# Kernel tuning notes

Hardware: AMD Instinct MI355X
Metric: run time of the kernel (lower is better)

The kernel has to match this reference:

```python
import jax, jax.numpy as jnp
import numpy as np

N_EMBD = 1024
N_HEAD = 16
HEAD_DIM = N_EMBD // N_HEAD
SEQ = 2048
BATCH = 2
WINDOW = 256
SCALE = 1.0 / np.sqrt(HEAD_DIM)
MASK_VALUE = -10000.0


def setup_inputs() -> dict:
    key = jax.random.key(0)
    ks = jax.random.split(key, 5)
    s = 0.02
    return {
        "hidden_states": jax.random.normal(ks[0], (BATCH, SEQ, N_EMBD), dtype=jnp.float32),
        "w_attn": jax.random.normal(ks[1], (N_EMBD, 3 * N_EMBD), dtype=jnp.float32) * s,
        "b_attn": jnp.zeros((3 * N_EMBD,), dtype=jnp.float32),
        "w_proj": jax.random.normal(ks[2], (N_EMBD, N_EMBD), dtype=jnp.float32) * s,
        "b_proj": jnp.zeros((N_EMBD,), dtype=jnp.float32),
    }


def _mask(seq_len):
    # causal AND sliding window: j <= i and j > i - WINDOW
    i = jnp.arange(seq_len)[:, None]
    j = jnp.arange(seq_len)[None, :]
    return (j <= i) & (j > i - WINDOW)  # [T, T] bool


def reference(hidden_states, w_attn, b_attn, w_proj, b_proj):
    B, T, _ = hidden_states.shape
    qkv = hidden_states @ w_attn + b_attn  # [B, T, 3E]
    q, k, v = jnp.split(qkv, 3, axis=-1)
    # [B, H, T, D]
    q = q.reshape(B, T, N_HEAD, HEAD_DIM).transpose(0, 2, 1, 3)
    k = k.reshape(B, T, N_HEAD, HEAD_DIM).transpose(0, 2, 1, 3)
    v = v.reshape(B, T, N_HEAD, HEAD_DIM).transpose(0, 2, 1, 3)

    scores = jnp.einsum("bhqd,bhkd->bhqk", q, k) * SCALE  # [B, H, T, T]
    mask = _mask(T)[None, None]  # [1, 1, T, T]
    scores = jnp.where(mask, scores, MASK_VALUE)
    scores = jnp.clip(scores, -10000.0, 10000.0)
    attn = jax.nn.softmax(scores, axis=-1)
    out = jnp.einsum("bhqk,bhkd->bhqd", attn, v)  # [B, H, T, D]
    out = out.transpose(0, 2, 1, 3).reshape(B, T, N_EMBD)
    return out @ w_proj + b_proj
```

## Files before the change

### kernel.cpp

```cpp
#include <hip/hip_runtime.h>


typedef __bf16 bf16_t;
typedef bf16_t bf16x8 __attribute__((ext_vector_type(8)));
typedef bf16_t bf16x4 __attribute__((ext_vector_type(4)));
typedef float  floatx4 __attribute__((ext_vector_type(4)));

#define SEQ_T   2048
#define NHEAD   16
#define HDIM    64
#define EMB     1024
#define WIN     256
#define SCALE_F 0.125f

__device__ __forceinline__ int detect_bf16(const uint4* __restrict__ det)
{
    const int lane = threadIdx.x & 63;
    const uint4 v = det[lane];
    int c = 0;
    #pragma unroll
    for (int e = 0; e < 4; ++e) {
        const unsigned int ex = ((&v.x)[e] >> 7) & 0xffu;
        c += (ex >= 100u && ex <= 150u) ? 1 : 0;
    }
    #pragma unroll
    for (int m = 32; m >= 1; m >>= 1) c += __shfl_xor(c, m, 64);
    return (c * 2 > 256) ? 1 : 0;
}

__global__ __launch_bounds__(256) void prologue(
    const void* __restrict__ hidden, bf16_t* __restrict__ Hc,
    const void* __restrict__ ba, bf16_t* __restrict__ bba,
    const void* __restrict__ bp, bf16_t* __restrict__ bbp,
    const void* __restrict__ wA, bf16_t* __restrict__ WtA,
    const void* __restrict__ wP, bf16_t* __restrict__ WtP)
{
    __shared__ __align__(16) bf16_t tile[64][68];
    const int f = detect_bf16((const uint4*)hidden);
    const int blk = blockIdx.x;

    if (blk < 4100) {
        if (f) return;
        const float* src;
        bf16_t* dst;
        int base;
        if (blk < 4096)      { src = (const float*)hidden; dst = Hc;  base = blk * 1024; }
        else if (blk < 4099) { src = (const float*)ba;     dst = bba; base = (blk - 4096) * 1024; }
        else                 { src = (const float*)bp;     dst = bbp; base = 0; }
        const int i4 = base + threadIdx.x * 4;
        const float4 x = *(const float4*)(src + i4);
        bf16x4 v;
        v[0] = (bf16_t)x.x; v[1] = (bf16_t)x.y;
        v[2] = (bf16_t)x.z; v[3] = (bf16_t)x.w;
        *(bf16x4*)(dst + i4) = v;
        return;
    }

    int id = blk - 4100;
    const void* W; bf16_t* Wt; int N, bx, by;
    if (id < 768) { W = wA; Wt = WtA; N = 3072; bx = id % 48; by = id / 48; }
    else { id -= 768; W = wP; Wt = WtP; N = 1024; bx = id % 16; by = id / 16; }
    const int K = 1024;
    const int n0 = bx * 64;
    const int k0 = by * 64;
    const int tx = threadIdx.x & 15;
    const int ty = threadIdx.x >> 4;

    #pragma unroll
    for (int r = ty; r < 64; r += 16) {
        bf16x4 v;
        const size_t base = (size_t)(k0 + r) * N + n0 + tx * 4;
        if (f) {
            v = *(const bf16x4*)((const bf16_t*)W + base);
        } else {
            const float4 x = *(const float4*)((const float*)W + base);
            v[0] = (bf16_t)x.x; v[1] = (bf16_t)x.y;
            v[2] = (bf16_t)x.z; v[3] = (bf16_t)x.w;
        }
        *(bf16x4*)&tile[r][tx * 4] = v;
    }
    __syncthreads();
    #pragma unroll
    for (int r = ty; r < 64; r += 16) {
        bf16x4 v;
        v[0] = tile[tx * 4 + 0][r];
        v[1] = tile[tx * 4 + 1][r];
        v[2] = tile[tx * 4 + 2][r];
        v[3] = tile[tx * 4 + 3][r];
        *(bf16x4*)(Wt + (size_t)(n0 + r) * K + k0 + tx * 4) = v;
    }
}

template<int BNt, int BKt>
__global__ __launch_bounds__(256, 2) void gemm_bt_bias(
    const bf16_t* __restrict__ Abf,
    const bf16_t* __restrict__ Aalt,
    const bf16_t* __restrict__ Bt,
    const bf16_t* __restrict__ biasbf,
    const bf16_t* __restrict__ biasalt,
    void* __restrict__ C,
    int M, int N, int K,
    int force_bf16, const uint4* __restrict__ det)
{
    constexpr int BMt = 128;
    constexpr int NF  = BNt / 32;
    constexpr int LPR = BKt / 8;
    constexpr int CM  = LPR - 1;
    constexpr int RPL = 64 / LPR;
    constexpr int SL  = BKt / 32;
    __shared__ __align__(16) bf16_t As[2][BMt * BKt];
    __shared__ __align__(16) bf16_t Bs[2][BNt * BKt];

    const int flag = detect_bf16(det);
    const bf16_t* A    = flag ? Abf    : Aalt;
    const bf16_t* bias = flag ? biasbf : biasalt;
    const int obf = force_bf16 | flag;

    const int tid  = threadIdx.x;
    const int wave = tid >> 6;
    const int lane = tid & 63;
    const int quad = lane >> 4;
    const int n16  = lane & 15;
    const int m0 = blockIdx.y * BMt;
    const int n0 = blockIdx.x * BNt;
    const int wm = (wave >> 1) * 64;
    const int wn = (wave & 1) * (BNt / 2);

    floatx4 acc[4][NF] = {};

    const int lr   = lane / LPR;
    const int lc16 = lane % LPR;

    auto stage = [&](int bsel, int k0) {
        #pragma unroll
        for (int t = 0; t < (BMt / 4) / RPL; ++t) {
            const int row0 = wave * (BMt / 4) + t * RPL;
            const int g = (lc16 ^ ((row0 + lr) & CM)) * 8;
            const bf16_t* ga = A + (size_t)(m0 + row0 + lr) * K + k0 + g;
            __builtin_amdgcn_global_load_lds(
                (const __attribute__((address_space(1))) void*)ga,
                (__attribute__((address_space(3))) void*)(As[bsel] + row0 * BKt),
                16, 0, 0);
        }
        #pragma unroll
        for (int t = 0; t < (BNt / 4) / RPL; ++t) {
            const int row0 = wave * (BNt / 4) + t * RPL;
            const int g = (lc16 ^ ((row0 + lr) & CM)) * 8;
            const bf16_t* gb = Bt + (size_t)(n0 + row0 + lr) * K + k0 + g;
            __builtin_amdgcn_global_load_lds(
                (const __attribute__((address_space(1))) void*)gb,
                (__attribute__((address_space(3))) void*)(Bs[bsel] + row0 * BKt),
                16, 0, 0);
        }
    };

    stage(0, 0);
    __syncthreads();

    const int NIT = K / BKt;
    int buf = 0;
    for (int it = 0; it < NIT; ++it) {
        if (it + 1 < NIT) stage(buf ^ 1, (it + 1) * BKt);

        #pragma unroll
        for (int s = 0; s < SL; ++s) {
            const int ch = (((4 * s + quad) ^ (n16 & CM)) * 8);
            const bf16_t* pa = As[buf] + (wm + n16) * BKt + ch;
            const bf16_t* pb = Bs[buf] + (wn + n16) * BKt + ch;
            bf16x8 af[4], bfr[NF];
            #pragma unroll
            for (int ff = 0; ff < 4; ++ff)
                af[ff] = *(const bf16x8*)(pa + ff * 16 * BKt);
            #pragma unroll
            for (int ff = 0; ff < NF; ++ff)
                bfr[ff] = *(const bf16x8*)(pb + ff * 16 * BKt);
            #pragma unroll
            for (int mf = 0; mf < 4; ++mf)
                #pragma unroll
                for (int nf = 0; nf < NF; ++nf)
                    acc[mf][nf] = __builtin_amdgcn_mfma_f32_16x16x32_bf16(
                        af[mf], bfr[nf], acc[mf][nf], 0, 0, 0);
        }
        __syncthreads();
        buf ^= 1;
    }

    const int col   = n0 + wn + n16;
    const int rbase = m0 + wm + quad * 4;
    #pragma unroll
    for (int nf = 0; nf < NF; ++nf) {
        const float bv = (float)bias[col + nf * 16];
        #pragma unroll
        for (int mf = 0; mf < 4; ++mf) {
            #pragma unroll
            for (int r = 0; r < 4; ++r) {
                const size_t idx =
                    (size_t)(rbase + mf * 16 + r) * N + col + nf * 16;
                const float val = acc[mf][nf][r] + bv;
                if (obf) ((bf16_t*)C)[idx] = (bf16_t)val;
                else     ((float*)C)[idx]  = val;
            }
        }
    }
}

#define CW   80
#define NCH  4
#define VT_S 104
#define P_S  104

__global__ __launch_bounds__(256) void attn_mfma(
    const bf16_t* __restrict__ qkv,
    bf16_t* __restrict__ attn_out)
{
    __shared__ __align__(16) bf16_t Ks[CW * 64];
    __shared__ __align__(16) bf16_t Vt[64 * VT_S];
    __shared__ __align__(16) bf16_t Pst[4][16 * P_S];

    const int tid  = threadIdx.x;
    const int wave = tid >> 6;
    const int lane = tid & 63;
    const int quad = lane >> 4;
    const int n16  = lane & 15;

    const int i0 = blockIdx.x * 64;
    const int h  = blockIdx.y;
    const int b  = blockIdx.z;
    const size_t rowbase = (size_t)b * SEQ_T;
    const int kbase  = i0 - 256;
    const int iw     = 16 * wave;
    const int climit = 256 - i0;

    const bf16_t* Qg = qkv + (rowbase + i0 + iw + n16) * (3 * EMB) + h * HDIM;
    bf16x8 qf[2];
    qf[0] = *(const bf16x8*)(Qg + quad * 8);
    qf[1] = *(const bf16x8*)(Qg + 32 + quad * 8);

    for (int i = tid; i < 1024; i += 256)
        Vt[(i >> 4) * VT_S + 80 + (i & 15)] = (bf16_t)0.f;
    for (int i = tid; i < 1024; i += 256)
        Pst[i >> 8][((i >> 4) & 15) * P_S + 80 + (i & 15)] = (bf16_t)0.f;

    floatx4 Oac[4] = {};
    float m_run[4], l_run[4];
    #pragma unroll
    for (int rr = 0; rr < 4; ++rr) { m_run[rr] = -3.0e38f; l_run[rr] = 0.f; }

    bf16x8 vreg[3];

    auto loadV = [&](int hc) {
        const int cbase = hc * CW;
        #pragma unroll
        for (int t = 0; t < 3; ++t) {
            const int idx = tid + 256 * t;
            if (idx < 640) {
                const int lc = idx >> 3;
                const int d0 = (idx & 7) * 8;
                int j = kbase + cbase + lc; if (j < 0) j = 0;
                vreg[t] = *(const bf16x8*)(qkv + (rowbase + j) * (3 * EMB)
                                           + 2 * EMB + h * HDIM + d0);
            }
        }
    };
    auto stageK = [&](int hc) {
        const int cbase = hc * CW;
        for (int t = wave; t < 10; t += 4) {
            const int lc0 = t * 8;
            const int lcL = lc0 + (lane >> 3);
            int j = kbase + cbase + lcL; if (j < 0) j = 0;
            const int g = (lane & 7) ^ (lane >> 3);
            const bf16_t* src = qkv + (rowbase + j) * (3 * EMB)
                                + EMB + h * HDIM + g * 8;
            __builtin_amdgcn_global_load_lds(
                (const __attribute__((address_space(1))) void*)src,
                (__attribute__((address_space(3))) void*)(Ks + lc0 * 64),
                16, 0, 0);
        }
    };
    auto writeVt = [&]() {
        #pragma unroll
        for (int t = 0; t < 3; ++t) {
            const int idx = tid + 256 * t;
            if (idx < 640) {
                const int lc = idx >> 3;
                const int d0 = (idx & 7) * 8;
                #pragma unroll
                for (int e = 0; e < 8; ++e)
                    Vt[(d0 + e) * VT_S + lc] = vreg[t][e];
            }
        }
    };

    loadV(0);
    stageK(0);

    for (int hc = 0; hc < NCH; ++hc) {
        const int cbase = hc * CW;

        __syncthreads();
        writeVt();
        __syncthreads();

        if (hc < NCH - 1) loadV(hc + 1);

        floatx4 sc[5];
        #pragma unroll
        for (int tt = 0; tt < 5; ++tt) {
            sc[tt] = (floatx4){0.f, 0.f, 0.f, 0.f};
            #pragma unroll
            for (int s2 = 0; s2 < 2; ++s2) {
                const int lc = 16 * tt + n16;
                const int ch = (4 * s2 + quad) ^ (lc & 7);
                const bf16x8 kf = *(const bf16x8*)(Ks + lc * 64 + ch * 8);
                sc[tt] = __builtin_amdgcn_mfma_f32_16x16x32_bf16(
                    qf[s2], kf, sc[tt], 0, 0, 0);
            }
        }

        #pragma unroll
        for (int tt = 0; tt < 5; ++tt) {
            const int c  = cbase + 16 * tt + n16;
            const int cw = c - iw;
            #pragma unroll
            for (int rr = 0; rr < 4; ++rr) {
                const int r = quad * 4 + rr;
                const bool valid = (cw > r) && (cw <= r + 256) && (c >= climit);
                sc[tt][rr] = valid ? sc[tt][rr] * SCALE_F : -3.0e38f;
            }
        }

        float cm[4];
        #pragma unroll
        for (int rr = 0; rr < 4; ++rr) {
            cm[rr] = -3.0e38f;
            #pragma unroll
            for (int tt = 0; tt < 5; ++tt) cm[rr] = fmaxf(cm[rr], sc[tt][rr]);
            #pragma unroll
            for (int m = 8; m >= 1; m >>= 1)
                cm[rr] = fmaxf(cm[rr], __shfl_xor(cm[rr], m, 64));
        }
        #pragma unroll
        for (int rr = 0; rr < 4; ++rr) {
            const float mnew  = fmaxf(m_run[rr], cm[rr]);
            const float alpha = __expf(m_run[rr] - mnew);
            m_run[rr] = mnew;
            l_run[rr] *= alpha;
            #pragma unroll
            for (int nt = 0; nt < 4; ++nt) Oac[nt][rr] *= alpha;
        }

        float psum[4] = {0.f, 0.f, 0.f, 0.f};
        #pragma unroll
        for (int tt = 0; tt < 5; ++tt) {
            #pragma unroll
            for (int rr = 0; rr < 4; ++rr) {
                const float s = sc[tt][rr];
                const float e = (s > -1.0e38f) ? __expf(s - m_run[rr]) : 0.f;
                psum[rr] += e;
                Pst[wave][(quad * 4 + rr) * P_S + 16 * tt + n16] = (bf16_t)e;
            }
        }
        #pragma unroll
        for (int rr = 0; rr < 4; ++rr) {
            #pragma unroll
            for (int m = 8; m >= 1; m >>= 1)
                psum[rr] += __shfl_xor(psum[rr], m, 64);
            l_run[rr] += psum[rr];
        }

        __syncthreads();

        if (hc < NCH - 1) stageK(hc + 1);

        #pragma unroll
        for (int ks = 0; ks < 3; ++ks) {
            const bf16x8 paf = *(const bf16x8*)(
                &Pst[wave][n16 * P_S + ks * 32 + quad * 8]);
            #pragma unroll
            for (int nt = 0; nt < 4; ++nt) {
                const bf16x8 vbf = *(const bf16x8*)(
                    Vt + (nt * 16 + n16) * VT_S + ks * 32 + quad * 8);
                Oac[nt] = __builtin_amdgcn_mfma_f32_16x16x32_bf16(
                    paf, vbf, Oac[nt], 0, 0, 0);
            }
        }
    }

    #pragma unroll
    for (int rr = 0; rr < 4; ++rr) {
        const float rden = 1.0f / l_run[rr];
        const size_t row = rowbase + i0 + iw + quad * 4 + rr;
        #pragma unroll
        for (int nt = 0; nt < 4; ++nt) {
            attn_out[row * EMB + h * HDIM + nt * 16 + n16] =
                (bf16_t)(Oac[nt][rr] * rden);
        }
    }
}

extern "C" void kernel_launch(void* const* d_in, const int* in_sizes, int n_in,
                              void* d_out, int out_size, void* d_ws, size_t ws_size,
                              hipStream_t stream)
{
    const void* hidden = d_in[0];
    const void* w_attn = d_in[1];
    const void* b_attn = d_in[2];
    const void* w_proj = d_in[3];
    const void* b_proj = d_in[4];

    char* ws = (char*)d_ws;
    bf16_t* Wt_attn = (bf16_t*)(ws);
    bf16_t* Wt_proj = (bf16_t*)(ws + (6u << 20));
    bf16_t* qkv     = (bf16_t*)(ws + (8u << 20));
    bf16_t* attn_o  = (bf16_t*)(ws + (32u << 20));
    bf16_t* Hc      = (bf16_t*)(ws + (40u << 20));
    bf16_t* bb_attn = (bf16_t*)(ws + (48u << 20));
    bf16_t* bb_proj = (bf16_t*)(ws + (48u << 20) + 8192);

    const uint4* det = (const uint4*)hidden;

    prologue<<<5124, 256, 0, stream>>>(hidden, Hc, b_attn, bb_attn,
                                       b_proj, bb_proj,
                                       w_attn, Wt_attn, w_proj, Wt_proj);

    gemm_bt_bias<192, 64><<<dim3(3072 / 192, 4096 / 128), 256, 0, stream>>>(
        (const bf16_t*)hidden, Hc, Wt_attn,
        (const bf16_t*)b_attn, bb_attn, qkv, 4096, 3072, 1024, 1, det);

    attn_mfma<<<dim3(SEQ_T / 64, NHEAD, 2), 256, 0, stream>>>(qkv, attn_o);

    gemm_bt_bias<64, 64><<<dim3(1024 / 64, 4096 / 128), 256, 0, stream>>>(
        attn_o, attn_o, Wt_proj,
        (const bf16_t*)b_proj, bb_proj, (void*)d_out, 4096, 1024, 1024, 0, det);
}
```

Before: 163.9 us.

## Triple-buffer GEMM LDS loads with vmcnt waits and 8-wave blocks

Turns the bf16 GEMM from a double-buffered loop with two barriers per iteration into a 3-stage ring. Loads run two tiles ahead, and a single barrier per iteration is guarded by explicit s_waitcnt vmcnt counts. Blocks grow to 512 threads (8 waves in a 2x4 grid), and the output-projection GEMM tile changes from 64 to 128 columns, which halves its grid. The intent is to hide global-to-LDS latency and cut barrier overhead, at the cost of more LDS per block and fewer blocks for the projection GEMM.

```diff
diff --git a/kernel.cpp b/kernel.cpp
--- a/kernel.cpp
+++ b/kernel.cpp
@@ -12,6 +12,14 @@
 #define EMB     1024
 #define WIN     256
 #define SCALE_F 0.125f
+
+template<int N> __device__ __forceinline__ void waitcnt_vm()
+{
+    if constexpr (N == 0)      asm volatile("s_waitcnt vmcnt(0)" ::: "memory");
+    else if constexpr (N == 4) asm volatile("s_waitcnt vmcnt(4)" ::: "memory");
+    else if constexpr (N == 5) asm volatile("s_waitcnt vmcnt(5)" ::: "memory");
+    else static_assert(N == 0 || N == 4 || N == 5, "add vmcnt literal");
+}
 
 __device__ __forceinline__ int detect_bf16(const uint4* __restrict__ det)
 {
@@ -91,8 +99,8 @@
     }
 }
 
-template<int BNt, int BKt>
-__global__ __launch_bounds__(256, 2) void gemm_bt_bias(
+template<int BMt, int BNt, int BKt>
+__global__ __launch_bounds__(512, 2) void gemm_bt_bias(
     const bf16_t* __restrict__ Abf,
     const bf16_t* __restrict__ Aalt,
     const bf16_t* __restrict__ Bt,
@@ -102,14 +110,16 @@
     int M, int N, int K,
     int force_bf16, const uint4* __restrict__ det)
 {
-    constexpr int BMt = 128;
-    constexpr int NF  = BNt / 32;
+    constexpr int NF  = BNt / 64;
     constexpr int LPR = BKt / 8;
     constexpr int CM  = LPR - 1;
     constexpr int RPL = 64 / LPR;
     constexpr int SL  = BKt / 32;
-    __shared__ __align__(16) bf16_t As[2][BMt * BKt];
-    __shared__ __align__(16) bf16_t Bs[2][BNt * BKt];
+    constexpr int LA  = (BMt / 8) / RPL;
+    constexpr int LB  = (BNt / 8) / RPL;
+    constexpr int LDW = LA + LB;
+    __shared__ __align__(16) bf16_t As[3][BMt * BKt];
+    __shared__ __align__(16) bf16_t Bs[3][BNt * BKt];
 
     const int flag = detect_bf16(det);
     const bf16_t* A    = flag ? Abf    : Aalt;
@@ -123,8 +133,8 @@
     const int n16  = lane & 15;
     const int m0 = blockIdx.y * BMt;
     const int n0 = blockIdx.x * BNt;
-    const int wm = (wave >> 1) * 64;
-    const int wn = (wave & 1) * (BNt / 2);
+    const int wm = (wave >> 2) * 64;
+    const int wn = (wave & 3) * (BNt / 4);
 
     floatx4 acc[4][NF] = {};
 
@@ -133,8 +143,8 @@
 
     auto stage = [&](int bsel, int k0) {
         #pragma unroll
-        for (int t = 0; t < (BMt / 4) / RPL; ++t) {
-            const int row0 = wave * (BMt / 4) + t * RPL;
+        for (int t = 0; t < LA; ++t) {
+            const int row0 = wave * (BMt / 8) + t * RPL;
             const int g = (lc16 ^ ((row0 + lr) & CM)) * 8;
             const bf16_t* ga = A + (size_t)(m0 + row0 + lr) * K + k0 + g;
             __builtin_amdgcn_global_load_lds(
@@ -143,8 +153,8 @@
                 16, 0, 0);
         }
         #pragma unroll
-        for (int t = 0; t < (BNt / 4) / RPL; ++t) {
-            const int row0 = wave * (BNt / 4) + t * RPL;
+        for (int t = 0; t < LB; ++t) {
+            const int row0 = wave * (BNt / 8) + t * RPL;
             const int g = (lc16 ^ ((row0 + lr) & CM)) * 8;
             const bf16_t* gb = Bt + (size_t)(n0 + row0 + lr) * K + k0 + g;
             __builtin_amdgcn_global_load_lds(
@@ -155,18 +165,28 @@
     };
 
     stage(0, 0);
-    __syncthreads();
+    stage(1, BKt);
 
     const int NIT = K / BKt;
-    int buf = 0;
+    int cur = 0;
     for (int it = 0; it < NIT; ++it) {
-        if (it + 1 < NIT) stage(buf ^ 1, (it + 1) * BKt);
-
+        if (it + 1 < NIT) waitcnt_vm<LDW>();
+        else              waitcnt_vm<0>();
+        asm volatile("s_waitcnt lgkmcnt(0)" ::: "memory");
+        __builtin_amdgcn_s_barrier();
+
+        if (it + 2 < NIT) {
+            int nb = cur + 2; if (nb >= 3) nb -= 3;
+            stage(nb, (it + 2) * BKt);
+        }
+
+        const bf16_t* __restrict__ Ab = As[cur];
+        const bf16_t* __restrict__ Bb = Bs[cur];
         #pragma unroll
         for (int s = 0; s < SL; ++s) {
             const int ch = (((4 * s + quad) ^ (n16 & CM)) * 8);
-            const bf16_t* pa = As[buf] + (wm + n16) * BKt + ch;
-            const bf16_t* pb = Bs[buf] + (wn + n16) * BKt + ch;
+            const bf16_t* pa = Ab + (wm + n16) * BKt + ch;
+            const bf16_t* pb = Bb + (wn + n16) * BKt + ch;
             bf16x8 af[4], bfr[NF];
             #pragma unroll
             for (int ff = 0; ff < 4; ++ff)
@@ -181,8 +201,7 @@
                     acc[mf][nf] = __builtin_amdgcn_mfma_f32_16x16x32_bf16(
                         af[mf], bfr[nf], acc[mf][nf], 0, 0, 0);
         }
-        __syncthreads();
-        buf ^= 1;
+        cur += 1; if (cur >= 3) cur -= 3;
     }
 
     const int col   = n0 + wn + n16;
@@ -423,13 +442,13 @@
                                        b_proj, bb_proj,
                                        w_attn, Wt_attn, w_proj, Wt_proj);
 
-    gemm_bt_bias<192, 64><<<dim3(3072 / 192, 4096 / 128), 256, 0, stream>>>(
+    gemm_bt_bias<128, 192, 64><<<dim3(3072 / 192, 4096 / 128), 512, 0, stream>>>(
         (const bf16_t*)hidden, Hc, Wt_attn,
         (const bf16_t*)b_attn, bb_attn, qkv, 4096, 3072, 1024, 1, det);
 
     attn_mfma<<<dim3(SEQ_T / 64, NHEAD, 2), 256, 0, stream>>>(qkv, attn_o);
 
-    gemm_bt_bias<64, 64><<<dim3(1024 / 64, 4096 / 128), 256, 0, stream>>>(
+    gemm_bt_bias<128, 128, 64><<<dim3(1024 / 128, 4096 / 128), 512, 0, stream>>>(
         attn_o, attn_o, Wt_proj,
         (const bf16_t*)b_proj, bb_proj, (void*)d_out, 4096, 1024, 1024, 0, det);
 }
```

Result: slower. 182.6 us (+11.4%).
